# Kernel optimization log

Measured on AMD Instinct MI355X. Metric: run time of the kernel, lower is better.

The kernel has to match this reference:

```python
import jax, jax.numpy as jnp
import numpy as np

EPS = 1e-5
N_HEAD = 8

def setup_inputs() -> dict:
    key = jax.random.key(0)
    ks = jax.random.split(key, 8)
    n, c, h, w = 8, 512, 64, 64
    feats_in = 512
    x = jax.random.normal(ks[0], (n, c, h, w), jnp.float32)
    cond = jax.random.normal(ks[1], (n, feats_in), jnp.float32)
    # AdaGN linear: feats_in -> 2*c
    W_ada = jax.random.normal(ks[2], (feats_in, 2 * c), jnp.float32) * (1.0 / np.sqrt(feats_in))
    b_ada = jnp.zeros((2 * c,), jnp.float32)
    # qkv 1x1 conv: c -> 3c
    W_qkv = jax.random.normal(ks[3], (3 * c, c), jnp.float32) * (1.0 / np.sqrt(c))
    b_qkv = jnp.zeros((3 * c,), jnp.float32)
    # out 1x1 conv: c -> c
    W_out = jax.random.normal(ks[4], (c, c), jnp.float32) * (1.0 / np.sqrt(c))
    b_out = jnp.zeros((c,), jnp.float32)
    return {"x": x, "cond": cond, "W_ada": W_ada, "b_ada": b_ada,
            "W_qkv": W_qkv, "b_qkv": b_qkv, "W_out": W_out, "b_out": b_out}

def reference(x, cond, W_ada, b_ada, W_qkv, b_qkv, W_out, b_out):
    n, c, h, w = x.shape
    nh = N_HEAD
    dh = c // nh
    s = h * w
    # AdaGN: GroupNorm with 1 group, no affine, then scale/shift from cond
    scales_shifts = cond @ W_ada + b_ada  # [n, 2c]
    scales, shifts = scales_shifts[:, :c], scales_shifts[:, c:]
    xf = x.reshape(n, -1)
    mean = xf.mean(axis=1, keepdims=True)
    var = xf.var(axis=1, keepdims=True)
    normed = ((xf - mean) * jax.lax.rsqrt(var + EPS)).reshape(n, c, h, w)
    normed = shifts[:, :, None, None] + normed * (scales[:, :, None, None] + 1.0)
    # qkv 1x1 conv
    qkv = jnp.einsum('nchw,oc->nohw', normed, W_qkv) + b_qkv[None, :, None, None]
    # view [n, nh*3, dh, s] then transpose -> [n, nh*3, s, dh]
    qkv = qkv.reshape(n, nh * 3, dh, s).transpose(0, 1, 3, 2)
    q, k, v = jnp.split(qkv, 3, axis=1)  # each [n, nh, s, dh]
    scale = dh ** (-0.25)
    att = jnp.einsum('nhsd,nhtd->nhst', q * scale, k * scale)
    att = jax.nn.softmax(att, axis=-1)
    y = jnp.einsum('nhst,nhtd->nhsd', att, v)  # [n, nh, s, dh]
    y = y.transpose(0, 1, 3, 2).reshape(n, c, h, w)
    out = jnp.einsum('nchw,oc->nohw', y, W_out) + b_out[None, :, None, None]
    return x + out
```

## Files before the change

kernel.cpp:

```cpp
#include <hip/hip_runtime.h>

#define NB   8
#define CC   512
#define SS   4096
#define NHD  8
#define DH   64
#define FEAT 512
#define NPER (CC*SS)

typedef unsigned short ushort_t;
typedef __attribute__((ext_vector_type(8))) short bf16x8;
typedef __attribute__((ext_vector_type(4))) float f32x4;

__device__ inline float b2f(ushort_t h) {
    union { unsigned int u; float f; } v; v.u = ((unsigned int)h) << 16; return v.f;
}
__device__ inline ushort_t f2b(float f) {
    union { float f; unsigned int u; } v; v.f = f;
    unsigned int u = v.u;
    u += 0x7fffu + ((u >> 16) & 1u);
    return (ushort_t)(u >> 16);
}
__device__ inline void unpack8(uint4 v, ushort_t* us) {
    us[0] = v.x & 0xffff; us[1] = v.x >> 16;
    us[2] = v.y & 0xffff; us[3] = v.y >> 16;
    us[4] = v.z & 0xffff; us[5] = v.z >> 16;
    us[6] = v.w & 0xffff; us[7] = v.w >> 16;
}
__device__ inline float loadIn(const void* p, size_t idx, int isf) {
    return isf ? ((const float*)p)[idx] : b2f(((const ushort_t*)p)[idx]);
}
__device__ inline void load8(const void* p, size_t idx, int isf, float* f) {
    if (isf) {
        const float* q = (const float*)p + idx;
        float4 a = *(const float4*)q, b = *(const float4*)(q + 4);
        f[0]=a.x; f[1]=a.y; f[2]=a.z; f[3]=a.w; f[4]=b.x; f[5]=b.y; f[6]=b.z; f[7]=b.w;
    } else {
        uint4 v = *(const uint4*)((const ushort_t*)p + idx);
        ushort_t us[8]; unpack8(v, us);
        for (int j = 0; j < 8; ++j) f[j] = b2f(us[j]);
    }
}
__device__ inline bf16x8 loadfrag(const void* p, size_t idx, int isf) {
    if (isf) {
        float f[8]; load8(p, idx, 1, f);
        bf16x8 r;
        for (int j = 0; j < 8; ++j) r[j] = (short)f2b(f[j]);
        return r;
    }
    union { uint4 u; bf16x8 v; } cvt;
    cvt.u = *(const uint4*)((const ushort_t*)p + idx);
    return cvt.v;
}

__global__ void probe_kernel(const unsigned int* __restrict__ x, int* __restrict__ flag) {
    unsigned int w = x[threadIdx.x & 63];
    unsigned int elo = (w >> 7) & 0xFF;
    int hit = (elo >= 0x60 && elo <= 0x9F) ? 1 : 0;
    for (int m = 1; m < 64; m <<= 1) hit += __shfl_xor(hit, m, 64);
    if (threadIdx.x == 0) *flag = (hit >= 40) ? 0 : 1;
}

__global__ __launch_bounds__(256) void ada_kernel(
    const void* __restrict__ cond, const void* __restrict__ W,
    const void* __restrict__ bias, float* __restrict__ out,
    const int* __restrict__ flagp)
{
    int isf = *flagp;
    int n = blockIdx.x;
    int j = blockIdx.y * 256 + threadIdx.x;
    float acc = loadIn(bias, j, isf);
    for (int k = 0; k < FEAT; ++k)
        acc += loadIn(cond, (size_t)n * FEAT + k, isf) * loadIn(W, (size_t)k * (2 * CC) + j, isf);
    out[n * (2 * CC) + j] = acc;
}

__global__ __launch_bounds__(256) void stats_kernel(
    const void* __restrict__ x, float* __restrict__ part, const int* __restrict__ flagp)
{
    int isf = *flagp;
    int n = blockIdx.x, blk = blockIdx.y;
    int tid = threadIdx.x;
    float s = 0.f, ss = 0.f;
    size_t base8 = (size_t)blk * 4096 + tid;
    for (int i = 0; i < 16; ++i) {
        float f[8];
        load8(x, ((size_t)n * NPER) + (base8 + (size_t)i * 256) * 8, isf, f);
        for (int j = 0; j < 8; ++j) { s += f[j]; ss += f[j] * f[j]; }
    }
    for (int m = 1; m < 64; m <<= 1) { s += __shfl_xor(s, m, 64); ss += __shfl_xor(ss, m, 64); }
    int w = tid >> 6;
    if ((tid & 63) == 0) {
        part[(size_t)n * 512 + (blk * 4 + w) * 2 + 0] = s;
        part[(size_t)n * 512 + (blk * 4 + w) * 2 + 1] = ss;
    }
}

__global__ __launch_bounds__(256) void coef_kernel(
    const float* __restrict__ ada, const float* __restrict__ part,
    float* __restrict__ coefA, float* __restrict__ coefB)
{
    __shared__ float reds[4], redss[4], mv[2];
    int n = blockIdx.x;
    int tid = threadIdx.x;
    float s  = part[(size_t)n * 512 + tid * 2 + 0];
    float ss = part[(size_t)n * 512 + tid * 2 + 1];
    for (int m = 1; m < 64; m <<= 1) { s += __shfl_xor(s, m, 64); ss += __shfl_xor(ss, m, 64); }
    int w = tid >> 6, lane = tid & 63;
    if (lane == 0) { reds[w] = s; redss[w] = ss; }
    __syncthreads();
    if (tid == 0) {
        float S  = (reds[0] + reds[1]) + (reds[2] + reds[3]);
        float S2 = (redss[0] + redss[1]) + (redss[2] + redss[3]);
        float inv = 1.f / (float)NPER;
        float mean = S * inv;
        float var  = S2 * inv - mean * mean;
        mv[0] = mean;
        mv[1] = rsqrtf(var + 1e-5f);
    }
    __syncthreads();
    float mean = mv[0], r = mv[1];
    int c = blockIdx.y * 256 + tid;
    float a = (ada[n * (2 * CC) + c] + 1.f) * r;
    coefA[n * CC + c] = a;
    coefB[n * CC + c] = ada[n * (2 * CC) + CC + c] - mean * a;
}

__global__ __launch_bounds__(256) void qkv_gemm_kernel(
    const void* __restrict__ A, const void* __restrict__ X, const void* __restrict__ bias,
    ushort_t* __restrict__ C,
    const float* __restrict__ coefA, const float* __restrict__ coefB,
    const int* __restrict__ flagp, int nb, int hb, int hc)
{
    __shared__ __align__(16) short Alds[64][72];
    __shared__ __align__(16) short Blds[64][72];
    int isf = *flagp;
    int z = blockIdx.z;
    int nIdx = nb + z;
    int yb = blockIdx.y;
    int p = yb / hc, hh = yb % hc;
    int arow0 = p * 512 + (hb + hh) * 64;
    size_t cbase = ((size_t)(z * 3 + p) * (hc * 64) + hh * 64) * SS;
    int n0 = blockIdx.x * 64;
    int tid = threadIdx.x;
    int w = tid >> 6, lane = tid & 63;
    int quad = lane >> 4, l16 = lane & 15;
    int wm = (w >> 1) * 32, wn = (w & 1) * 32;
    f32x4 acc[2][2] = {};

    for (int k0 = 0; k0 < 512; k0 += 64) {
        __syncthreads();
        for (int it = 0; it < 2; ++it) {
            int chunk = tid + it * 256;
            int row = chunk >> 3, cb = chunk & 7;
            float f[8];
            load8(A, (size_t)(arow0 + row) * 512 + k0 + cb * 8, isf, f);
            short o[8];
            for (int j = 0; j < 8; ++j) o[j] = (short)f2b(f[j]);
            *(uint4*)&Alds[row][cb * 8] = *(uint4*)o;
        }
        for (int it = 0; it < 2; ++it) {
            int chunk = tid + it * 256;
            int c = chunk >> 3, hb8 = chunk & 7;
            int ch = k0 + c;
            float f[8];
            load8(X, (size_t)nIdx * NPER + (size_t)ch * SS + n0 + hb8 * 8, isf, f);
            float a = coefA[nIdx * CC + ch], b = coefB[nIdx * CC + ch];
            for (int j = 0; j < 8; ++j)
                Blds[hb8 * 8 + j][c] = (short)f2b(a * f[j] + b);
        }
        __syncthreads();
        for (int kk = 0; kk < 2; ++kk) {
            bf16x8 af[2], bfv[2];
            for (int mi = 0; mi < 2; ++mi)
                af[mi] = *(const bf16x8*)&Alds[wm + mi * 16 + l16][kk * 32 + quad * 8];
            for (int ni = 0; ni < 2; ++ni)
                bfv[ni] = *(const bf16x8*)&Blds[wn + ni * 16 + l16][kk * 32 + quad * 8];
            for (int mi = 0; mi < 2; ++mi)
                for (int ni = 0; ni < 2; ++ni)
                    acc[mi][ni] = __builtin_amdgcn_mfma_f32_16x16x32_bf16(
                        af[mi], bfv[ni], acc[mi][ni], 0, 0, 0);
        }
    }
    if (p < 2) {
        const float SCL = 0.42467078f;
        for (int mi = 0; mi < 2; ++mi)
            for (int ni = 0; ni < 2; ++ni) {
                int col = n0 + wn + ni * 16 + l16;
                int d0 = wm + mi * 16 + quad * 4;
                ushort_t pk[4];
                for (int r = 0; r < 4; ++r) {
                    float v = (acc[mi][ni][r] + loadIn(bias, arow0 + d0 + r, isf)) * SCL;
                    pk[r] = f2b(v);
                }
                *(ushort4*)&C[cbase + (size_t)col * 64 + d0] =
                    make_ushort4(pk[0], pk[1], pk[2], pk[3]);
            }
    } else {
        for (int mi = 0; mi < 2; ++mi)
            for (int ni = 0; ni < 2; ++ni) {
                int col = n0 + wn + ni * 16 + l16;
                for (int r = 0; r < 4; ++r) {
                    int rowl = wm + mi * 16 + quad * 4 + r;
                    float v = acc[mi][ni][r] + loadIn(bias, arow0 + rowl, isf);
                    C[cbase + (size_t)rowl * SS + col] = f2b(v);
                }
            }
    }
}

__global__ __launch_bounds__(256, 4) void attn_kernel(
    const ushort_t* __restrict__ qkv,
    ushort_t* __restrict__ y,
    int nb, int hb, int hc)
{
    __shared__ __align__(16) short Klds[64][64];
    __shared__ __align__(16) short Vlds[64][64];
    __shared__ __align__(16) short Plds[4][32][64];

    int s0 = blockIdx.x * 128;
    int hl = blockIdx.y;
    int z = blockIdx.z;
    int n = nb + z;
    int hcc = hc * 64;
    const ushort_t* Q = qkv + ((size_t)(z * 3 + 0) * hcc + hl * 64) * SS;
    const ushort_t* K = qkv + ((size_t)(z * 3 + 1) * hcc + hl * 64) * SS;
    const ushort_t* V = qkv + ((size_t)(z * 3 + 2) * hcc + hl * 64) * SS;

    int tid = threadIdx.x;
    int w = tid >> 6, lane = tid & 63;
    int quad = lane >> 4, l16 = lane & 15;
    int sw = l16 & 7;

    bf16x8 qf[2][2];
    for (int si = 0; si < 2; ++si)
        for (int kk = 0; kk < 2; ++kk)
            qf[si][kk] = *(const bf16x8*)&Q[(size_t)(s0 + w * 32 + si * 16 + l16) * 64
                                            + kk * 32 + quad * 8];

    const short ONE = 0x3F80;
    bf16x8 ones = { ONE, ONE, ONE, ONE, ONE, ONE, ONE, ONE };

    f32x4 o[2][4] = {};
    f32x4 sum_acc[2] = {};

    for (int t0 = 0; t0 < SS; t0 += 64) {
        __syncthreads();
        for (int it = 0; it < 2; ++it) {
            int chunk = tid + it * 256;
            int row = chunk >> 3, cb = chunk & 7;
            int cw = (cb ^ (row & 7)) * 8;
            *(uint4*)&Klds[row][cw] = *(const uint4*)&K[(size_t)(t0 + row) * 64 + cb * 8];
            *(uint4*)&Vlds[row][cw] = *(const uint4*)&V[(size_t)row * SS + t0 + cb * 8];
        }
        __syncthreads();

        for (int nt = 0; nt < 4; ++nt) {
            f32x4 sA = { -16.f, -16.f, -16.f, -16.f };
            f32x4 sB = { -16.f, -16.f, -16.f, -16.f };
            for (int kk = 0; kk < 2; ++kk) {
                bf16x8 kf = *(const bf16x8*)&Klds[nt * 16 + l16][((kk * 4 + quad) ^ sw) * 8];
                sA = __builtin_amdgcn_mfma_f32_16x16x32_bf16(qf[0][kk], kf, sA, 0, 0, 0);
                sB = __builtin_amdgcn_mfma_f32_16x16x32_bf16(qf[1][kk], kf, sB, 0, 0, 0);
            }
            for (int r = 0; r < 4; ++r) {
                float pA = exp2f(sA[r]);
                float pB = exp2f(sB[r]);
                int srow = quad * 4 + r;
                int chunk = ((nt * 2 + (l16 >> 3)) ^ (srow & 7)) * 8 + (l16 & 7);
                Plds[w][srow][chunk]      = (short)(__float_as_uint(pA) >> 16);
                Plds[w][16 + srow][chunk] = (short)(__float_as_uint(pB) >> 16);
            }
        }

        for (int kk = 0; kk < 2; ++kk) {
            bf16x8 vf[4];
            for (int dt = 0; dt < 4; ++dt)
                vf[dt] = *(const bf16x8*)&Vlds[dt * 16 + l16][((kk * 4 + quad) ^ sw) * 8];
            for (int si = 0; si < 2; ++si) {
                bf16x8 pf = *(const bf16x8*)&Plds[w][si * 16 + l16][((kk * 4 + quad) ^ sw) * 8];
                sum_acc[si] = __builtin_amdgcn_mfma_f32_16x16x32_bf16(pf, ones, sum_acc[si], 0, 0, 0);
                for (int dt = 0; dt < 4; ++dt)
                    o[si][dt] = __builtin_amdgcn_mfma_f32_16x16x32_bf16(pf, vf[dt], o[si][dt], 0, 0, 0);
            }
        }
    }

    for (int si = 0; si < 2; ++si) {
        f32x4 inv;
        for (int r = 0; r < 4; ++r) inv[r] = 1.0f / sum_acc[si][r];
        for (int dt = 0; dt < 4; ++dt) {
            int d = dt * 16 + l16;
            int cidx = (hb + hl) * DH + d;
            size_t bidx = ((size_t)n * CC + cidx) * SS + s0 + w * 32 + si * 16 + quad * 4;
            ushort_t pk[4];
            for (int r = 0; r < 4; ++r) pk[r] = f2b(o[si][dt][r] * inv[r]);
            *(ushort4*)&y[bidx] = make_ushort4(pk[0], pk[1], pk[2], pk[3]);
        }
    }
}

__global__ __launch_bounds__(512) void out_gemm_kernel(
    const void* __restrict__ W, const void* __restrict__ bias, const void* __restrict__ x,
    const ushort_t* __restrict__ ybuf, float* __restrict__ out,
    const int* __restrict__ flagp)
{
    __shared__ __align__(16) short Ylds[64][264];
    int isf = *flagp;
    int n = blockIdx.y;
    int s0 = blockIdx.x * 64;
    int tid = threadIdx.x;
    int w = tid >> 6, lane = tid & 63;
    int quad = lane >> 4, l16 = lane & 15;
    const ushort_t* Yb = ybuf + (size_t)n * ((size_t)CC * SS);
    float* Op = out + (size_t)n * NPER;

    f32x4 acc[4][4] = {};
    for (int kh = 0; kh < 2; ++kh) {
        __syncthreads();
        int ch = (tid & 255) + kh * 256;
        int cg = tid >> 8;
        for (int cb = 0; cb < 4; ++cb) {
            uint4 v = *(const uint4*)&Yb[(size_t)ch * SS + s0 + cg * 32 + cb * 8];
            ushort_t us[8]; unpack8(v, us);
            for (int j = 0; j < 8; ++j) Ylds[cg * 32 + cb * 8 + j][tid & 255] = (short)us[j];
        }
        __syncthreads();
        for (int k0 = 0; k0 < 256; k0 += 32) {
            bf16x8 af[4];
            for (int mi = 0; mi < 4; ++mi)
                af[mi] = loadfrag(W, (size_t)(w * 64 + mi * 16 + l16) * 512 + kh * 256 + k0 + quad * 8, isf);
            for (int ni = 0; ni < 4; ++ni) {
                bf16x8 bfv = *(const bf16x8*)&Ylds[ni * 16 + l16][k0 + quad * 8];
                for (int mi = 0; mi < 4; ++mi)
                    acc[mi][ni] = __builtin_amdgcn_mfma_f32_16x16x32_bf16(
                        af[mi], bfv, acc[mi][ni], 0, 0, 0);
            }
        }
    }

    for (int mi = 0; mi < 4; ++mi)
        for (int ni = 0; ni < 4; ++ni) {
            int col = s0 + ni * 16 + l16;
            for (int r = 0; r < 4; ++r) {
                int m = w * 64 + mi * 16 + quad * 4 + r;
                size_t idx = (size_t)m * SS + col;
                float v = acc[mi][ni][r] + loadIn(bias, m, isf)
                        + loadIn(x, (size_t)n * NPER + idx, isf);
                Op[idx] = v;
            }
        }
}

extern "C" void kernel_launch(void* const* d_in, const int* in_sizes, int n_in,
                              void* d_out, int out_size, void* d_ws, size_t ws_size,
                              hipStream_t stream) {
    (void)in_sizes; (void)n_in; (void)out_size;
    const void* x     = d_in[0];
    const void* cond  = d_in[1];
    const void* W_ada = d_in[2];
    const void* b_ada = d_in[3];
    const void* W_qkv = d_in[4];
    const void* b_qkv = d_in[5];
    const void* W_out = d_in[6];
    const void* b_out = d_in[7];
    float* out = (float*)d_out;

    char* ws = (char*)d_ws;
    float* part  = (float*)ws;
    float* ada   = (float*)(ws + 16384);
    float* coefA = (float*)(ws + 49152);
    float* coefB = (float*)(ws + 65536);
    int*   flag  = (int*)(ws + 81920);
    ushort_t* ybuf   = (ushort_t*)(ws + 82176);
    const size_t BASE = 82176ULL + (size_t)NB * NPER * 2;
    ushort_t* qkvbuf = (ushort_t*)(ws + BASE);

    const size_t PER_HS = (size_t)3 * 64 * SS * 2;
    size_t avail = ws_size > BASE ? ws_size - BASE : 0;
    int NC = 1, HC = 1;
    if      (avail >= 64 * PER_HS) { NC = 8; HC = 8; }
    else if (avail >= 32 * PER_HS) { NC = 4; HC = 8; }
    else if (avail >= 16 * PER_HS) { NC = 2; HC = 8; }
    else if (avail >=  8 * PER_HS) { NC = 1; HC = 8; }
    else if (avail >=  4 * PER_HS) { NC = 1; HC = 4; }
    else if (avail >=  2 * PER_HS) { NC = 1; HC = 2; }

    probe_kernel<<<1, 64, 0, stream>>>((const unsigned int*)x, flag);
    ada_kernel  <<<dim3(NB, 4),  256, 0, stream>>>(cond, W_ada, b_ada, ada, flag);
    stats_kernel<<<dim3(NB, 64), 256, 0, stream>>>(x, part, flag);
    coef_kernel <<<dim3(NB, 2),  256, 0, stream>>>(ada, part, coefA, coefB);

    for (int nb = 0; nb < NB; nb += NC)
        for (int hb = 0; hb < NHD; hb += HC) {
            qkv_gemm_kernel<<<dim3(64, 3 * HC, NC), 256, 0, stream>>>(
                W_qkv, x, b_qkv, qkvbuf, coefA, coefB, flag, nb, hb, HC);
            attn_kernel<<<dim3(32, HC, NC), 256, 0, stream>>>(
                qkvbuf, ybuf, nb, hb, HC);
        }

    out_gemm_kernel<<<dim3(64, NB), 512, 0, stream>>>(W_out, b_out, x, ybuf, out, flag);
}
```

Baseline: 952.0 us.

## Keep attention probabilities in registers via permlane swaps instead of LDS

Computes S transposed (K as the A operand, Q as B) so each lane holds scores laid out for the P·V MFMA operand. The bf16 probabilities are packed with v_cvt_pk_bf16_f32 and redistributed with permlane32/16 swaps, removing the per-warp Plds LDS buffer and its write/read round trip. QK and PV work are also interleaved per kk chunk. This cuts LDS traffic and LDS footprint, in exchange for inline asm that relies on gfx950 permlane instructions and changes rounding (round-to-nearest instead of truncation).

```diff
diff --git a/kernel.cpp b/kernel.cpp
--- a/kernel.cpp
+++ b/kernel.cpp
@@ -216,7 +216,6 @@
 {
     __shared__ __align__(16) short Klds[64][64];
     __shared__ __align__(16) short Vlds[64][64];
-    __shared__ __align__(16) short Plds[4][32][64];
 
     int s0 = blockIdx.x * 128;
     int hl = blockIdx.y;
@@ -255,33 +254,44 @@
         }
         __syncthreads();
 
-        for (int nt = 0; nt < 4; ++nt) {
-            f32x4 sA = { -16.f, -16.f, -16.f, -16.f };
-            f32x4 sB = { -16.f, -16.f, -16.f, -16.f };
-            for (int kk = 0; kk < 2; ++kk) {
-                bf16x8 kf = *(const bf16x8*)&Klds[nt * 16 + l16][((kk * 4 + quad) ^ sw) * 8];
-                sA = __builtin_amdgcn_mfma_f32_16x16x32_bf16(qf[0][kk], kf, sA, 0, 0, 0);
-                sB = __builtin_amdgcn_mfma_f32_16x16x32_bf16(qf[1][kk], kf, sB, 0, 0, 0);
-            }
-            for (int r = 0; r < 4; ++r) {
-                float pA = exp2f(sA[r]);
-                float pB = exp2f(sB[r]);
-                int srow = quad * 4 + r;
-                int chunk = ((nt * 2 + (l16 >> 3)) ^ (srow & 7)) * 8 + (l16 & 7);
-                Plds[w][srow][chunk]      = (short)(__float_as_uint(pA) >> 16);
-                Plds[w][16 + srow][chunk] = (short)(__float_as_uint(pB) >> 16);
-            }
-        }
-
         for (int kk = 0; kk < 2; ++kk) {
+            f32x4 sv[2][2];
+            for (int ntl = 0; ntl < 2; ++ntl) {
+                int nt = kk * 2 + ntl;
+                bf16x8 kf0 = *(const bf16x8*)&Klds[nt * 16 + l16][((0 * 4 + quad) ^ sw) * 8];
+                bf16x8 kf1 = *(const bf16x8*)&Klds[nt * 16 + l16][((1 * 4 + quad) ^ sw) * 8];
+                for (int si = 0; si < 2; ++si) {
+                    f32x4 a = { -16.f, -16.f, -16.f, -16.f };
+                    a = __builtin_amdgcn_mfma_f32_16x16x32_bf16(kf0, qf[si][0], a, 0, 0, 0);
+                    a = __builtin_amdgcn_mfma_f32_16x16x32_bf16(kf1, qf[si][1], a, 0, 0, 0);
+                    sv[ntl][si] = a;
+                }
+            }
+
             bf16x8 vf[4];
             for (int dt = 0; dt < 4; ++dt)
                 vf[dt] = *(const bf16x8*)&Vlds[dt * 16 + l16][((kk * 4 + quad) ^ sw) * 8];
+
             for (int si = 0; si < 2; ++si) {
-                bf16x8 pf = *(const bf16x8*)&Plds[w][si * 16 + l16][((kk * 4 + quad) ^ sw) * 8];
-                sum_acc[si] = __builtin_amdgcn_mfma_f32_16x16x32_bf16(pf, ones, sum_acc[si], 0, 0, 0);
+                float p0 = exp2f(sv[0][si][0]), p1 = exp2f(sv[0][si][1]);
+                float p2 = exp2f(sv[0][si][2]), p3 = exp2f(sv[0][si][3]);
+                float p4 = exp2f(sv[1][si][0]), p5 = exp2f(sv[1][si][1]);
+                float p6 = exp2f(sv[1][si][2]), p7 = exp2f(sv[1][si][3]);
+                unsigned int x0, x1, y0, y1;
+                asm("v_cvt_pk_bf16_f32 %0, %1, %2" : "=v"(x0) : "v"(p0), "v"(p1));
+                asm("v_cvt_pk_bf16_f32 %0, %1, %2" : "=v"(x1) : "v"(p2), "v"(p3));
+                asm("v_cvt_pk_bf16_f32 %0, %1, %2" : "=v"(y0) : "v"(p4), "v"(p5));
+                asm("v_cvt_pk_bf16_f32 %0, %1, %2" : "=v"(y1) : "v"(p6), "v"(p7));
+                asm("v_permlane32_swap_b32 %0, %1" : "+v"(x0), "+v"(y0));
+                asm("v_permlane32_swap_b32 %0, %1" : "+v"(x1), "+v"(y1));
+                asm("v_permlane16_swap_b32 %0, %1" : "+v"(x0), "+v"(y0));
+                asm("v_permlane16_swap_b32 %0, %1" : "+v"(x1), "+v"(y1));
+                union { unsigned int u[4]; bf16x8 v; } frag;
+                frag.u[0] = x0; frag.u[1] = x1; frag.u[2] = y0; frag.u[3] = y1;
+
+                sum_acc[si] = __builtin_amdgcn_mfma_f32_16x16x32_bf16(frag.v, ones, sum_acc[si], 0, 0, 0);
                 for (int dt = 0; dt < 4; ++dt)
-                    o[si][dt] = __builtin_amdgcn_mfma_f32_16x16x32_bf16(pf, vf[dt], o[si][dt], 0, 0, 0);
+                    o[si][dt] = __builtin_amdgcn_mfma_f32_16x16x32_bf16(frag.v, vf[dt], o[si][dt], 0, 0, 0);
             }
         }
     }
```

New measurement: 927.6 us. 1.03x faster.
